# Performance work log

Hardware: AMD Instinct MI355X
Metric: run time of the kernel (lower is better)

Reference implementation:

```python
import jax, jax.numpy as jnp
import numpy as np

N_ITEM = 100000
D = 512
CODEBOOK = 2048
B = 2048
K = 200
PAD = 0


def setup_inputs() -> dict:
    key = jax.random.key(0)
    ks = jax.random.split(key, 10)
    user_id = jax.random.randint(ks[0], (B,), 0, 100000)
    interacted_items = jax.random.randint(ks[1], (B, K), 0, N_ITEM + 1)
    pos = jax.random.randint(ks[2], (B,), 0, N_ITEM + 1)
    neg = jax.random.randint(ks[3], (B,), 0, N_ITEM + 1)
    item_embed = jax.random.normal(ks[4], (N_ITEM + 1, D), dtype=jnp.float32) * 0.01
    # map MLP: latent_dim -> 2*latent_dim -> latent_dim (PyTorch default init scale-ish)
    W1 = jax.random.normal(ks[5], (D, 2 * D), dtype=jnp.float32) * (1.0 / np.sqrt(D))
    b1 = jnp.zeros((2 * D,), dtype=jnp.float32)
    W2 = jax.random.normal(ks[6], (2 * D, D), dtype=jnp.float32) * (1.0 / np.sqrt(2 * D))
    b2 = jnp.zeros((D,), dtype=jnp.float32)
    codebook = jax.random.normal(ks[7], (CODEBOOK, D), dtype=jnp.float32)
    return {
        "user_id": user_id,
        "interacted_items": interacted_items,
        "pos": pos,
        "neg": neg,
        "item_embed": item_embed,
        "W1": W1,
        "b1": b1,
        "W2": W2,
        "b2": b2,
        "codebook": codebook,
    }


def reference(user_id, interacted_items, pos, neg, item_embed, W1, b1, W2, b2, codebook):
    # mask out padding, masked mean over history (user_embed_method == 'item')
    keep = (interacted_items != PAD).astype(item_embed.dtype)[..., None]  # [B,K,1]
    hist = item_embed[interacted_items]                                   # [B,K,D]
    mean_item = jnp.sum(hist * keep, axis=1) / jnp.sum(keep, axis=1)      # [B,D]
    # map MLP
    user_embed = jax.nn.relu(mean_item @ W1 + b1) @ W2 + b2               # [B,D]
    # VQ quantize (eval mode: no EMA update): squared-distance argmin dispatch
    d2 = (
        jnp.sum(user_embed * user_embed, axis=1, keepdims=True)
        - 2.0 * user_embed @ codebook.T
        + jnp.sum(codebook * codebook, axis=1)[None, :]
    )                                                                     # [B,CODEBOOK]
    id_t = jnp.argmin(d2, axis=1)                                         # [B]
    q = codebook[id_t]                                                    # [B,D]
    diff = jnp.mean((jax.lax.stop_gradient(q) - user_embed) ** 2)         # scalar commitment loss
    quant_user = user_embed + jax.lax.stop_gradient(q - user_embed)       # straight-through
    pos_item = item_embed[pos]                                            # [B,D]
    neg_item = item_embed[neg]                                            # [B,D]
    return (quant_user, pos_item, neg_item, diff, user_embed)
```

## Files before the change

### kernel.cpp

```cpp
#include <hip/hip_runtime.h>

typedef unsigned short u16;
typedef unsigned long long u64;
typedef __attribute__((ext_vector_type(8))) short short8;
typedef __attribute__((ext_vector_type(4))) float f32x4;

#define B_ 2048
#define D_ 512
#define CB_ 2048
#define K_ 200

__device__ __forceinline__ u16 f2bf_rne(float f) {
    unsigned u = __float_as_uint(f);
    unsigned r = (u + 0x7fffu + ((u >> 16) & 1u)) >> 16;
    return (u16)r;
}

__device__ __forceinline__ u64 shfl_xor_u64(u64 v, int m) {
    int lo = __shfl_xor((int)(v & 0xffffffffu), m);
    int hi = __shfl_xor((int)(v >> 32), m);
    return ((u64)(unsigned)hi << 32) | (unsigned)lo;
}

__global__ void cbprep_kernel(const float* __restrict__ cb, u16* __restrict__ ch,
                              float* __restrict__ cnormf, float* __restrict__ diffacc) {
    __shared__ double red[128];
    int j = blockIdx.x, t = threadIdx.x;
    float4 v = ((const float4*)(cb + (size_t)j * D_))[t];
    ushort4 o;
    o.x = f2bf_rne(v.x); o.y = f2bf_rne(v.y); o.z = f2bf_rne(v.z); o.w = f2bf_rne(v.w);
    ((ushort4*)(ch + (size_t)j * D_))[t] = o;
    red[t] = (double)v.x * v.x + (double)v.y * v.y + (double)v.z * v.z + (double)v.w * v.w;
    __syncthreads();
    for (int s = 64; s > 0; s >>= 1) {
        if (t < s) red[t] += red[t + s];
        __syncthreads();
    }
    if (t == 0) {
        cnormf[j] = (float)red[0];
        if (j == 0) diffacc[0] = 0.0f;
    }
}

__global__ void transpose_w(const float* __restrict__ W, u16* __restrict__ WT, int K, int N) {
    __shared__ float tile[32][33];
    int n0 = blockIdx.x * 32, k0 = blockIdx.y * 32;
    int t = threadIdx.x;
    int kl = t >> 3, nl = (t & 7) * 4;
    float4 v = *(const float4*)(W + (size_t)(k0 + kl) * N + n0 + nl);
    tile[kl][nl] = v.x; tile[kl][nl + 1] = v.y; tile[kl][nl + 2] = v.z; tile[kl][nl + 3] = v.w;
    __syncthreads();
    int nl2 = t >> 3, kl2 = (t & 7) * 4;
    ushort4 o;
    o.x = f2bf_rne(tile[kl2][nl2]);
    o.y = f2bf_rne(tile[kl2 + 1][nl2]);
    o.z = f2bf_rne(tile[kl2 + 2][nl2]);
    o.w = f2bf_rne(tile[kl2 + 3][nl2]);
    *(ushort4*)(WT + (size_t)(n0 + nl2) * K + k0 + kl2) = o;
}

__global__ void mean_kernel(const int* __restrict__ items,
                            const float* __restrict__ item_embed,
                            u16* __restrict__ meanb) {
    __shared__ int sidx[K_];
    __shared__ float4 rs4[128];
    __shared__ int rc;
    int b = blockIdx.x, t = threadIdx.x;
    for (int k = t; k < K_; k += 256) sidx[k] = items[b * K_ + k];
    __syncthreads();
    int team = t >> 7;
    int lt = t & 127;
    int c = lt * 4;
    float s0 = 0.f, s1 = 0.f, s2 = 0.f, s3 = 0.f;
    int cnt = 0;
    int k0 = team * (K_ / 2);
#pragma unroll 4
    for (int k = k0; k < k0 + K_ / 2; k++) {
        int idx = sidx[k];
        float m = (idx != 0) ? 1.0f : 0.0f;
        cnt += (idx != 0) ? 1 : 0;
        float4 v = *(const float4*)(item_embed + (size_t)idx * D_ + c);
        s0 += v.x * m; s1 += v.y * m; s2 += v.z * m; s3 += v.w * m;
    }
    if (team == 1) {
        float4 p; p.x = s0; p.y = s1; p.z = s2; p.w = s3;
        rs4[lt] = p;
        if (lt == 0) rc = cnt;
    }
    __syncthreads();
    if (team == 0) {
        float4 p = rs4[lt];
        s0 += p.x; s1 += p.y; s2 += p.z; s3 += p.w;
        cnt += rc;
        float inv = 1.0f / (float)cnt;
        ushort4 o;
        o.x = f2bf_rne(s0 * inv); o.y = f2bf_rne(s1 * inv);
        o.z = f2bf_rne(s2 * inv); o.w = f2bf_rne(s3 * inv);
        *(ushort4*)(meanb + (size_t)b * D_ + c) = o;
    }
}

__global__ void gemm1_mfma(const u16* __restrict__ meanb, const u16* __restrict__ W1T,
                           const float* __restrict__ b1w, u16* __restrict__ hb) {
    int t = threadIdx.x;
    int wid = blockIdx.x * 4 + (t >> 6);
    int lane = t & 63;
    int mt = wid >> 5, nt = wid & 31;
    int m0 = mt * 16, n0 = nt * 32;
    int mr = lane & 15, quad = lane >> 4, kb = quad * 8;
    const u16* ap  = meanb + (size_t)(m0 + mr) * 512 + kb;
    const u16* bp0 = W1T + (size_t)(n0 + mr) * 512 + kb;
    const u16* bp1 = bp0 + 16 * 512;
    f32x4 acc0 = {0.f, 0.f, 0.f, 0.f}, acc1 = {0.f, 0.f, 0.f, 0.f};
#pragma unroll
    for (int ks = 0; ks < 16; ks++) {
        short8 a  = *(const short8*)(ap  + ks * 32);
        short8 b0 = *(const short8*)(bp0 + ks * 32);
        short8 b1 = *(const short8*)(bp1 + ks * 32);
        acc0 = __builtin_amdgcn_mfma_f32_16x16x32_bf16(a, b0, acc0, 0, 0, 0);
        acc1 = __builtin_amdgcn_mfma_f32_16x16x32_bf16(a, b1, acc1, 0, 0, 0);
    }
    float bias0 = b1w[n0 + mr], bias1 = b1w[n0 + 16 + mr];
#pragma unroll
    for (int r = 0; r < 4; r++) {
        int m = m0 + quad * 4 + r;
        float v0 = acc0[r] + bias0; v0 = v0 > 0.f ? v0 : 0.f;
        float v1 = acc1[r] + bias1; v1 = v1 > 0.f ? v1 : 0.f;
        hb[(size_t)m * 1024 + n0 + mr]      = f2bf_rne(v0);
        hb[(size_t)m * 1024 + n0 + 16 + mr] = f2bf_rne(v1);
    }
}

__global__ void gemm2_mfma(const u16* __restrict__ hb, const u16* __restrict__ W2T,
                           const float* __restrict__ b2w,
                           float* __restrict__ out_ue, u16* __restrict__ uh) {
    int t = threadIdx.x;
    int wid = blockIdx.x * 4 + (t >> 6);
    int lane = t & 63;
    int mt = wid >> 5, nt = wid & 31;
    int m0 = mt * 16, n0 = nt * 16;
    int mr = lane & 15, quad = lane >> 4, kb = quad * 8;
    const u16* ap = hb  + (size_t)(m0 + mr) * 1024 + kb;
    const u16* bp = W2T + (size_t)(n0 + mr) * 1024 + kb;
    f32x4 acc0 = {0.f, 0.f, 0.f, 0.f}, acc1 = {0.f, 0.f, 0.f, 0.f};
#pragma unroll
    for (int ks = 0; ks < 16; ks++) {
        short8 a0 = *(const short8*)(ap + ks * 32);
        short8 b0 = *(const short8*)(bp + ks * 32);
        short8 a1 = *(const short8*)(ap + 512 + ks * 32);
        short8 b1 = *(const short8*)(bp + 512 + ks * 32);
        acc0 = __builtin_amdgcn_mfma_f32_16x16x32_bf16(a0, b0, acc0, 0, 0, 0);
        acc1 = __builtin_amdgcn_mfma_f32_16x16x32_bf16(a1, b1, acc1, 0, 0, 0);
    }
    float bias = b2w[n0 + mr];
#pragma unroll
    for (int r = 0; r < 4; r++) {
        int m = m0 + quad * 4 + r;
        float v = acc0[r] + acc1[r] + bias;
        size_t o = (size_t)m * 512 + n0 + mr;
        out_ue[o] = v;
        uh[o] = f2bf_rne(v);
    }
}

__global__ void score_mfma(const u16* __restrict__ uh,
                           const u16* __restrict__ ch,
                           const float* __restrict__ cnormf,
                           u64* __restrict__ pminS) {
    __shared__ u64 red2[64];
    int t = threadIdx.x, lane = t & 63, w = t >> 6;
    int ustrip = blockIdx.x >> 3, jstrip = blockIdx.x & 7;
    int u0 = ustrip * 16;
    int j0 = jstrip * 256 + w * 64;
    int mr = lane & 15, quad = lane >> 4, kb = quad * 8;

    short8 af[16];
    const u16* ap = uh + (size_t)(u0 + mr) * 512 + kb;
#pragma unroll
    for (int ks = 0; ks < 16; ks++) af[ks] = *(const short8*)(ap + ks * 32);

    u64 best[4] = {~0ull, ~0ull, ~0ull, ~0ull};
    for (int jt = 0; jt < 4; jt++) {
        int jb = j0 + jt * 16;
        const u16* bp = ch + (size_t)(jb + mr) * 512 + kb;
        f32x4 acc = {0.f, 0.f, 0.f, 0.f};
#pragma unroll
        for (int ks = 0; ks < 16; ks++) {
            short8 bv = *(const short8*)(bp + ks * 32);
            acc = __builtin_amdgcn_mfma_f32_16x16x32_bf16(af[ks], bv, acc, 0, 0, 0);
        }
        int n = jb + mr;
        float cn = cnormf[n];
#pragma unroll
        for (int r = 0; r < 4; r++) {
            float d2 = cn - 2.0f * acc[r];
            u64 p = (((u64)__float_as_uint(d2)) << 32) | (unsigned)n;
            if (p < best[r]) best[r] = p;
        }
    }
#pragma unroll
    for (int off = 8; off >= 1; off >>= 1)
#pragma unroll
        for (int r = 0; r < 4; r++) {
            u64 o = shfl_xor_u64(best[r], off);
            if (o < best[r]) best[r] = o;
        }
    if (mr == 0) {
#pragma unroll
        for (int r = 0; r < 4; r++) red2[w * 16 + quad * 4 + r] = best[r];
    }
    __syncthreads();
    if (t < 16) {
        u64 m = red2[t];
#pragma unroll
        for (int ww = 1; ww < 4; ww++) {
            u64 v = red2[ww * 16 + t];
            if (v < m) m = v;
        }
        pminS[(size_t)(u0 + t) * 8 + jstrip] = m;
    }
}

__global__ void finalize_user(const u64* __restrict__ pminS,
                              const float* __restrict__ ub,
                              const float* __restrict__ cb,
                              float* __restrict__ out0,
                              float* __restrict__ diffacc) {
    __shared__ u64 sm64[8];
    __shared__ unsigned sbest;
    __shared__ float red[256];
    int b = blockIdx.x, t = threadIdx.x;
    if (t < 8) sm64[t] = pminS[(size_t)b * 8 + t];
    __syncthreads();
    if (t == 0) {
        u64 m = sm64[0];
#pragma unroll
        for (int i = 1; i < 8; i++) if (sm64[i] < m) m = sm64[i];
        sbest = (unsigned)(m & 0xffffffffu);
    }
    __syncthreads();
    unsigned bestj = sbest;
    int c = t * 2;
    float2 qv = ((const float2*)(cb + (size_t)bestj * 512))[t];
    float w0 = ub[(size_t)b * 512 + c];
    float w1 = ub[(size_t)b * 512 + c + 1];
    float2 o;
    o.x = w0 + (qv.x - w0);
    o.y = w1 + (qv.y - w1);
    ((float2*)(out0 + (size_t)b * 512))[t] = o;
    float d0 = qv.x - w0, d1 = qv.y - w1;
    red[t] = d0 * d0 + d1 * d1;
    __syncthreads();
    for (int s = 128; s > 0; s >>= 1) {
        if (t < s) red[t] += red[t + s];
        __syncthreads();
    }
    if (t == 0) atomicAdd(diffacc, red[0]);
}

__global__ void gather_pn(const int* __restrict__ pos, const int* __restrict__ neg,
                          const float* __restrict__ ie,
                          float* __restrict__ out1, float* __restrict__ out2) {
    int b = blockIdx.x, t = threadIdx.x;
    int p = pos[b], n = neg[b];
    ((float4*)(out1 + (size_t)b * 512))[t] = ((const float4*)(ie + (size_t)p * 512))[t];
    ((float4*)(out2 + (size_t)b * 512))[t] = ((const float4*)(ie + (size_t)n * 512))[t];
}

__global__ void diff_final(const float* __restrict__ diffacc, float* __restrict__ out3) {
    if (threadIdx.x == 0)
        out3[0] = diffacc[0] * (1.0f / ((float)B_ * (float)D_));
}

extern "C" void kernel_launch(void* const* d_in, const int* in_sizes, int n_in,
                              void* d_out, int out_size, void* d_ws, size_t ws_size,
                              hipStream_t stream) {
    const int* items = (const int*)d_in[1];
    const int* pos   = (const int*)d_in[2];
    const int* neg   = (const int*)d_in[3];
    const float* item_embed = (const float*)d_in[4];
    const float* W1 = (const float*)d_in[5];
    const float* b1 = (const float*)d_in[6];
    const float* W2 = (const float*)d_in[7];
    const float* b2 = (const float*)d_in[8];
    const float* cb = (const float*)d_in[9];

    float* out0 = (float*)d_out;
    float* out1 = out0 + (size_t)B_ * D_;
    float* out2 = out1 + (size_t)B_ * D_;
    float* out3 = out2 + (size_t)B_ * D_;
    float* out4 = out3 + 1;

    u16* hb = (u16*)out1;

    char* wsb = (char*)d_ws;
    u16* meanb = (u16*)wsb;
    u16* W1T   = (u16*)(wsb + 2097152);
    u16* W2T   = (u16*)(wsb + 3145728);
    u16* uh    = (u16*)(wsb + 4194304);
    u16* ch    = (u16*)(wsb + 6291456);
    u64* pminS = (u64*)(wsb + 8388608);
    float* cnormf  = (float*)(wsb + 8519680);
    float* diffacc = (float*)(wsb + 8527872);

    cbprep_kernel<<<dim3(CB_), dim3(128), 0, stream>>>(cb, ch, cnormf, diffacc);
    transpose_w<<<dim3(32, 16), dim3(256), 0, stream>>>(W1, W1T, 512, 1024);
    transpose_w<<<dim3(16, 32), dim3(256), 0, stream>>>(W2, W2T, 1024, 512);
    mean_kernel<<<dim3(B_), dim3(256), 0, stream>>>(items, item_embed, meanb);
    gemm1_mfma<<<dim3(1024), dim3(256), 0, stream>>>(meanb, W1T, b1, hb);
    gemm2_mfma<<<dim3(1024), dim3(256), 0, stream>>>(hb, W2T, b2, out4, uh);
    score_mfma<<<dim3(1024), dim3(256), 0, stream>>>(uh, ch, cnormf, pminS);
    finalize_user<<<dim3(B_), dim3(256), 0, stream>>>(pminS, out4, cb, out0, diffacc);
    gather_pn<<<dim3(B_), dim3(128), 0, stream>>>(pos, neg, item_embed, out1, out2);
    diff_final<<<dim3(1), dim3(64), 0, stream>>>(diffacc, out3);
}
```

Before: 499.3 us.

## Convert item embeddings to bf16 before history gather-mean

Adds a pass converting the full item embedding table to bf16 in workspace, then performs the history gather and mean on bf16 rows with 8-wide loads and four teams. Padding is handled by summing all rows and subtracting the pad row times its count, removing per-item masking. This halves gather bytes but adds a full-table conversion read and write every call, and is only used when the workspace is large enough.

After: 506.6 us. Within noise of the previous version (+1.5%).

```diff
diff --git a/kernel.cpp b/kernel.cpp
--- a/kernel.cpp
+++ b/kernel.cpp
@@ -9,11 +9,16 @@
 #define D_ 512
 #define CB_ 2048
 #define K_ 200
+#define NITEM_ 100001
 
 __device__ __forceinline__ u16 f2bf_rne(float f) {
     unsigned u = __float_as_uint(f);
     unsigned r = (u + 0x7fffu + ((u >> 16) & 1u)) >> 16;
     return (u16)r;
+}
+
+__device__ __forceinline__ float bf2f(u16 h) {
+    return __uint_as_float(((unsigned)h) << 16);
 }
 
 __device__ __forceinline__ u64 shfl_xor_u64(u64 v, int m) {
@@ -59,9 +64,67 @@
     *(ushort4*)(WT + (size_t)(n0 + nl2) * K + k0 + kl2) = o;
 }
 
-__global__ void mean_kernel(const int* __restrict__ items,
-                            const float* __restrict__ item_embed,
-                            u16* __restrict__ meanb) {
+__global__ void ie2bf_kernel(const float* __restrict__ ie, u16* __restrict__ iebf) {
+    const size_t n4 = (size_t)NITEM_ * D_ / 4;
+    for (size_t i = (size_t)blockIdx.x * 256 + threadIdx.x; i < n4;
+         i += (size_t)gridDim.x * 256) {
+        float4 v = ((const float4*)ie)[i];
+        ushort4 o;
+        o.x = f2bf_rne(v.x); o.y = f2bf_rne(v.y);
+        o.z = f2bf_rne(v.z); o.w = f2bf_rne(v.w);
+        ((ushort4*)iebf)[i] = o;
+    }
+}
+
+__global__ void mean_kernel_bf(const int* __restrict__ items,
+                               const u16* __restrict__ iebf,
+                               u16* __restrict__ meanb) {
+    __shared__ int sidx[K_];
+    __shared__ float rs[3][64][8];
+    __shared__ int rn[4];
+    int b = blockIdx.x, t = threadIdx.x;
+    for (int k = t; k < K_; k += 256) sidx[k] = items[b * K_ + k];
+    __syncthreads();
+    int team = t >> 6;
+    int lt = t & 63;
+    int c = lt * 8;
+    float s[8] = {0.f, 0.f, 0.f, 0.f, 0.f, 0.f, 0.f, 0.f};
+    int n0 = 0;
+    int k0 = team * (K_ / 4);
+#pragma unroll 4
+    for (int k = k0; k < k0 + K_ / 4; k++) {
+        int idx = sidx[k];
+        n0 += (idx == 0) ? 1 : 0;
+        short8 v = *(const short8*)(iebf + (size_t)idx * D_ + c);
+#pragma unroll
+        for (int e = 0; e < 8; e++) s[e] += bf2f((u16)v[e]);
+    }
+    if (team > 0) {
+#pragma unroll
+        for (int e = 0; e < 8; e++) rs[team - 1][lt][e] = s[e];
+    }
+    if (lt == 0) rn[team] = n0;
+    __syncthreads();
+    if (team == 0) {
+#pragma unroll
+        for (int tm = 0; tm < 3; tm++)
+#pragma unroll
+            for (int e = 0; e < 8; e++) s[e] += rs[tm][lt][e];
+        int n0t = rn[0] + rn[1] + rn[2] + rn[3];
+        float inv = 1.0f / (float)(K_ - n0t);
+        short8 r0 = *(const short8*)(iebf + c);
+        float fn0 = (float)n0t;
+        short8 o;
+#pragma unroll
+        for (int e = 0; e < 8; e++)
+            o[e] = (short)f2bf_rne((s[e] - fn0 * bf2f((u16)r0[e])) * inv);
+        *(short8*)(meanb + (size_t)b * D_ + c) = o;
+    }
+}
+
+__global__ void mean_kernel_f32(const int* __restrict__ items,
+                                const float* __restrict__ item_embed,
+                                u16* __restrict__ meanb) {
     __shared__ int sidx[K_];
     __shared__ float4 rs4[128];
     __shared__ int rc;
@@ -302,11 +365,19 @@
     u64* pminS = (u64*)(wsb + 8388608);
     float* cnormf  = (float*)(wsb + 8519680);
     float* diffacc = (float*)(wsb + 8527872);
+    u16* iebf      = (u16*)(wsb + 8650752);
+    const size_t WS_NEED_BF = 8650752ull + (size_t)NITEM_ * D_ * 2;
+    const bool use_bf = (ws_size >= WS_NEED_BF);
 
     cbprep_kernel<<<dim3(CB_), dim3(128), 0, stream>>>(cb, ch, cnormf, diffacc);
     transpose_w<<<dim3(32, 16), dim3(256), 0, stream>>>(W1, W1T, 512, 1024);
     transpose_w<<<dim3(16, 32), dim3(256), 0, stream>>>(W2, W2T, 1024, 512);
-    mean_kernel<<<dim3(B_), dim3(256), 0, stream>>>(items, item_embed, meanb);
+    if (use_bf) {
+        ie2bf_kernel<<<dim3(2048), dim3(256), 0, stream>>>(item_embed, iebf);
+        mean_kernel_bf<<<dim3(B_), dim3(256), 0, stream>>>(items, iebf, meanb);
+    } else {
+        mean_kernel_f32<<<dim3(B_), dim3(256), 0, stream>>>(items, item_embed, meanb);
+    }
     gemm1_mfma<<<dim3(1024), dim3(256), 0, stream>>>(meanb, W1T, b1, hb);
     gemm2_mfma<<<dim3(1024), dim3(256), 0, stream>>>(hb, W2T, b2, out4, uh);
     score_mfma<<<dim3(1024), dim3(256), 0, stream>>>(uh, ch, cnormf, pminS);
```

## Quantize item embeddings to int8 per row before gathered history mean

Applied to the files above, without the earlier changes.

Adds a pass that converts the whole item embedding table to int8 with a per-row scale, then computes the masked history mean from the int8 table. Padding rows are handled by subtracting the decoded row-0 contribution times the pad count. The aim is to shrink the bytes moved by the random gathers, but the full-table conversion reads all 200 MB every call and writes a 51 MB copy, which likely outweighs the gather savings (about 210 MB of fp32 rows). Precision also drops to int8, and the new path runs only when the workspace is large enough.

Measured after the change: 475.4 us. 4.8% less time.

```diff
diff --git a/kernel.cpp b/kernel.cpp
--- a/kernel.cpp
+++ b/kernel.cpp
@@ -9,6 +9,7 @@
 #define D_ 512
 #define CB_ 2048
 #define K_ 200
+#define NITEM_ 100001
 
 __device__ __forceinline__ u16 f2bf_rne(float f) {
     unsigned u = __float_as_uint(f);
@@ -20,6 +21,28 @@
     int lo = __shfl_xor((int)(v & 0xffffffffu), m);
     int hi = __shfl_xor((int)(v >> 32), m);
     return ((u64)(unsigned)hi << 32) | (unsigned)lo;
+}
+
+__device__ __forceinline__ void dec16_acc(uint4 qv, float sc, float* s) {
+    unsigned w[4] = {qv.x, qv.y, qv.z, qv.w};
+#pragma unroll
+    for (int j = 0; j < 4; j++) {
+        s[4 * j + 0] += (float)((int)(w[j] << 24) >> 24) * sc;
+        s[4 * j + 1] += (float)((int)(w[j] << 16) >> 24) * sc;
+        s[4 * j + 2] += (float)((int)(w[j] <<  8) >> 24) * sc;
+        s[4 * j + 3] += (float)((int)w[j] >> 24) * sc;
+    }
+}
+
+__device__ __forceinline__ void dec16_set(uint4 qv, float sc, float* r) {
+    unsigned w[4] = {qv.x, qv.y, qv.z, qv.w};
+#pragma unroll
+    for (int j = 0; j < 4; j++) {
+        r[4 * j + 0] = (float)((int)(w[j] << 24) >> 24) * sc;
+        r[4 * j + 1] = (float)((int)(w[j] << 16) >> 24) * sc;
+        r[4 * j + 2] = (float)((int)(w[j] <<  8) >> 24) * sc;
+        r[4 * j + 3] = (float)((int)w[j] >> 24) * sc;
+    }
 }
 
 __global__ void cbprep_kernel(const float* __restrict__ cb, u16* __restrict__ ch,
@@ -59,9 +82,107 @@
     *(ushort4*)(WT + (size_t)(n0 + nl2) * K + k0 + kl2) = o;
 }
 
-__global__ void mean_kernel(const int* __restrict__ items,
-                            const float* __restrict__ item_embed,
-                            u16* __restrict__ meanb) {
+__global__ void ie2q8_kernel(const float* __restrict__ ie, char* __restrict__ q8,
+                             float* __restrict__ scales) {
+    int gw = (blockIdx.x * 256 + threadIdx.x) >> 6;
+    int lane = threadIdx.x & 63;
+    int half = lane >> 5, hl = lane & 31;
+    int nw = (gridDim.x * 256) >> 6;
+    for (int base = gw * 2; base < NITEM_; base += nw * 2) {
+        int row = base + half;
+        if (row >= NITEM_) row = NITEM_ - 1;
+        const float* rp = ie + (size_t)row * D_ + hl * 16;
+        float4 a0 = *(const float4*)rp;
+        float4 a1 = *(const float4*)(rp + 4);
+        float4 a2 = *(const float4*)(rp + 8);
+        float4 a3 = *(const float4*)(rp + 12);
+        float f[16] = {a0.x, a0.y, a0.z, a0.w, a1.x, a1.y, a1.z, a1.w,
+                       a2.x, a2.y, a2.z, a2.w, a3.x, a3.y, a3.z, a3.w};
+        float m = 0.f;
+#pragma unroll
+        for (int e = 0; e < 16; e++) m = fmaxf(m, fabsf(f[e]));
+#pragma unroll
+        for (int off = 16; off >= 1; off >>= 1)
+            m = fmaxf(m, __shfl_xor(m, off));
+        float inv = (m > 0.f) ? 127.0f / m : 0.f;
+        float s = m * (1.0f / 127.0f);
+        unsigned w[4];
+#pragma unroll
+        for (int j = 0; j < 4; j++) {
+            int q0 = __float2int_rn(f[4 * j + 0] * inv) & 255;
+            int q1 = __float2int_rn(f[4 * j + 1] * inv) & 255;
+            int q2 = __float2int_rn(f[4 * j + 2] * inv) & 255;
+            int q3 = __float2int_rn(f[4 * j + 3] * inv) & 255;
+            w[j] = (unsigned)(q0 | (q1 << 8) | (q2 << 16) | (q3 << 24));
+        }
+        uint4 o; o.x = w[0]; o.y = w[1]; o.z = w[2]; o.w = w[3];
+        *(uint4*)(q8 + (size_t)row * D_ + hl * 16) = o;
+        if (hl == 0) scales[row] = s;
+    }
+}
+
+__global__ void mean_kernel_q8(const int* __restrict__ items,
+                               const char* __restrict__ q8,
+                               const float* __restrict__ scales,
+                               u16* __restrict__ meanb) {
+    __shared__ int sidx[K_];
+    __shared__ float rs[3][32][16];
+    __shared__ int rn_[4];
+    int b = blockIdx.x, t = threadIdx.x;
+    for (int k = t; k < K_; k += 256) sidx[k] = items[b * K_ + k];
+    __syncthreads();
+    int team = t >> 6;
+    int lane = t & 63;
+    int half = lane >> 5, hl = lane & 31;
+    int co = hl * 16;
+    float s[16];
+#pragma unroll
+    for (int e = 0; e < 16; e++) s[e] = 0.f;
+    int n0 = 0;
+    int k0 = team * (K_ / 4);
+#pragma unroll 5
+    for (int i = 0; i < K_ / 8; i++) {
+        int idx = sidx[k0 + 2 * i + half];
+        n0 += (idx == 0) ? 1 : 0;
+        float sc = scales[idx];
+        uint4 qv = *(const uint4*)(q8 + (size_t)idx * D_ + co);
+        dec16_acc(qv, sc, s);
+    }
+#pragma unroll
+    for (int e = 0; e < 16; e++) s[e] += __shfl_xor(s[e], 32);
+    n0 += __shfl_xor(n0, 32);
+    if (team > 0 && half == 0) {
+#pragma unroll
+        for (int e = 0; e < 16; e++) rs[team - 1][hl][e] = s[e];
+    }
+    if (lane == 0) rn_[team] = n0;
+    __syncthreads();
+    if (team == 0 && half == 0) {
+#pragma unroll
+        for (int tm = 0; tm < 3; tm++)
+#pragma unroll
+            for (int e = 0; e < 16; e++) s[e] += rs[tm][hl][e];
+        int n0t = rn_[0] + rn_[1] + rn_[2] + rn_[3];
+        float inv = 1.0f / (float)(K_ - n0t);
+        float fn0 = (float)n0t;
+        float s0 = scales[0];
+        uint4 q0 = *(const uint4*)(q8 + co);
+        float r0[16];
+        dec16_set(q0, s0, r0);
+        short8 o0, o1;
+#pragma unroll
+        for (int e = 0; e < 8; e++) {
+            o0[e] = (short)f2bf_rne((s[e] - fn0 * r0[e]) * inv);
+            o1[e] = (short)f2bf_rne((s[e + 8] - fn0 * r0[e + 8]) * inv);
+        }
+        *(short8*)(meanb + (size_t)b * D_ + co) = o0;
+        *(short8*)(meanb + (size_t)b * D_ + co + 8) = o1;
+    }
+}
+
+__global__ void mean_kernel_f32(const int* __restrict__ items,
+                                const float* __restrict__ item_embed,
+                                u16* __restrict__ meanb) {
     __shared__ int sidx[K_];
     __shared__ float4 rs4[128];
     __shared__ int rc;
@@ -302,11 +423,20 @@
     u64* pminS = (u64*)(wsb + 8388608);
     float* cnormf  = (float*)(wsb + 8519680);
     float* diffacc = (float*)(wsb + 8527872);
+    char*  iq8     = (char*)(wsb + 8650752);
+    float* iscal   = (float*)(wsb + 8650752 + 51200512);
+    const size_t WS_NEED_Q8 = 8650752ull + 51200512ull + 400004ull;
+    const bool use_q8 = (ws_size >= WS_NEED_Q8);
 
     cbprep_kernel<<<dim3(CB_), dim3(128), 0, stream>>>(cb, ch, cnormf, diffacc);
     transpose_w<<<dim3(32, 16), dim3(256), 0, stream>>>(W1, W1T, 512, 1024);
     transpose_w<<<dim3(16, 32), dim3(256), 0, stream>>>(W2, W2T, 1024, 512);
-    mean_kernel<<<dim3(B_), dim3(256), 0, stream>>>(items, item_embed, meanb);
+    if (use_q8) {
+        ie2q8_kernel<<<dim3(2048), dim3(256), 0, stream>>>(item_embed, iq8, iscal);
+        mean_kernel_q8<<<dim3(B_), dim3(256), 0, stream>>>(items, iq8, iscal, meanb);
+    } else {
+        mean_kernel_f32<<<dim3(B_), dim3(256), 0, stream>>>(items, item_embed, meanb);
+    }
     gemm1_mfma<<<dim3(1024), dim3(256), 0, stream>>>(meanb, W1T, b1, hb);
     gemm2_mfma<<<dim3(1024), dim3(256), 0, stream>>>(hb, W2T, b2, out4, uh);
     score_mfma<<<dim3(1024), dim3(256), 0, stream>>>(uh, ch, cnormf, pminS);
```
